# Optimization experiments

Measured on AMD Instinct MI355X. Metric: run time of the kernel, lower is better.

## Reference

```python
import jax, jax.numpy as jnp
import numpy as np

FPS, MS = 7, 256
WIDTHS = [(FPS, 12), (12, 12), (12, 12), (12, 12), (12, 12), (12, 6), (6, 1)]


def setup_inputs() -> dict:
    key = jax.random.key(0)
    keys = jax.random.split(key, 1 + 2 * len(WIDTHS))
    B = 32768
    inp = {"inputs": jax.random.normal(keys[0], (B, MS, FPS), dtype=jnp.float32)}
    for li, (fan_in, fan_out) in enumerate(WIDTHS):
        scale = 1.0 / np.sqrt(fan_in)
        inp[f"W{li}"] = jax.random.uniform(keys[1 + 2 * li], (fan_in, fan_out), dtype=jnp.float32, minval=-scale, maxval=scale)
        inp[f"b{li}"] = jnp.zeros((fan_out,), dtype=jnp.float32)
    return inp


def _mlp(x, Ws, bs):
    # layer 0: linear activation
    h = x @ Ws[0] + bs[0]
    # layers 1-4: relu
    for li in range(1, 5):
        h = jax.nn.relu(h @ Ws[li] + bs[li])
    # layer 5: linear (6 units), layer 6: final linear (1 unit)
    h = h @ Ws[5] + bs[5]
    h = h @ Ws[6] + bs[6]
    return h


def reference(inputs, W0, b0, W1, b1, W2, b2, W3, b3, W4, b4, W5, b5, W6, b6):
    B = inputs.shape[0]
    Ws = [W0, W1, W2, W3, W4, W5, W6]
    bs = [b0, b1, b2, b3, b4, b5, b6]
    # Equivalent to looping over ms slices with the shared MLP then concatenating:
    # fold the ms dim into the batch, run once, reshape back to [B, ms].
    x = inputs.reshape(B * MS, FPS)
    out = _mlp(x, Ws, bs)  # [B*MS, 1]
    return out.reshape(B, MS)
```

## Files before the change

kernel.cpp:

```cpp
#include <hip/hip_runtime.h>
#include <stdint.h>

typedef _Float16 half8  __attribute__((ext_vector_type(8)));
typedef __fp16   fp16x2 __attribute__((ext_vector_type(2)));
typedef float    floatx4 __attribute__((ext_vector_type(4)));
typedef uint32_t u32x4  __attribute__((ext_vector_type(4)));
typedef float    f4a    __attribute__((ext_vector_type(4), aligned(4)));

union FragU { u32x4 v; uint32_t u[4]; half8 h; };
union H2U   { fp16x2 h; uint32_t u; };
union FU    { float f; uint32_t u; };

#define NT 256
#define NBLOCKS 1024
#define NWAVES (NBLOCKS * (NT / 64))
#define ROWS_PER_GITER (NWAVES * 64)

__device__ __forceinline__ uint32_t splitpk(float y) {
    FU a; a.f = y; a.u &= 0xFFFFE000u;
    H2U r; r.h = __builtin_amdgcn_cvt_pkrtz(a.f, y - a.f);
    return r.u;
}

__global__ void build_frags(const float* __restrict__ W0, const float* __restrict__ b0,
                            const float* __restrict__ W1, const float* __restrict__ b1,
                            const float* __restrict__ W2, const float* __restrict__ b2,
                            const float* __restrict__ W3, const float* __restrict__ b3,
                            const float* __restrict__ W4, const float* __restrict__ b4,
                            const float* __restrict__ W5, const float* __restrict__ b5,
                            const float* __restrict__ W6, const float* __restrict__ b6,
                            uint32_t* __restrict__ ws)
{
    const int l = threadIdx.x;
    if (l >= 64) return;
    const int m = l & 15, g = l >> 4;
    const float* Wm[5] = {W0, W1, W2, W3, W4};
    const float* bm[5] = {b0, b1, b2, b3, b4};

    for (int s = 0; s < 6; ++s) {
        const int fan_in = (s == 0) ? 7 : 12;
        const int mmax   = (s == 5) ? 1 : 12;
        const float wscale = (s == 0) ? 64.0f : (s == 5 ? (1.0f / 64.0f) : 1.0f);
        for (int w = 0; w < 4; ++w) {
            const int i = g * 4 + w;
            uint32_t u1 = 0, u2 = 0;
            if (g == 3 && w == 3) {
                float bv = 0.0f;
                if (m < mmax) {
                    if (s == 5) { bv = b6[0]; for (int c = 0; c < 6; ++c) bv = fmaf(b5[c], W6[c], bv); }
                    else        { bv = 64.0f * bm[s][m]; }
                }
                H2U hh; hh.h = __builtin_amdgcn_cvt_pkrtz(bv, 0.0f);
                float hf = (float)hh.h[0];
                H2U ll; ll.h = __builtin_amdgcn_cvt_pkrtz(bv - hf, 0.0f);
                u1 = hh.u; u2 = ll.u;
            } else if (i < fan_in && m < mmax) {
                float wv;
                if (s == 5) { wv = 0.0f; for (int c = 0; c < 6; ++c) wv = fmaf(W5[i * 6 + c], W6[c], wv); wv *= wscale; }
                else        { wv = Wm[s][i * 12 + m] * wscale; }
                H2U hh; hh.h = __builtin_amdgcn_cvt_pkrtz(wv, wv);
                float hf = (float)hh.h[0];
                H2U ll; ll.h = __builtin_amdgcn_cvt_pkrtz(wv - hf, 0.0f);
                u1 = hh.u; u2 = ll.u;
            }
            ws[((s * 2 + 0) * 64 + l) * 4 + w] = u1;
            ws[((s * 2 + 1) * 64 + l) * 4 + w] = u2;
        }
    }
}

__device__ __forceinline__ void mlp16x4(const half8 (&A)[6][2], const f4a (&q)[4],
                                        floatx4 (&acc)[4], bool godd, bool g3)
{
    FragU B[4];
    #pragma unroll
    for (int st = 0; st < 4; ++st) {
        float v0 = godd ? (float)q[st][1] : (float)q[st][0];
        float v1 = godd ? (float)q[st][2] : (float)q[st][1];
        float v2 = godd ? (float)q[st][3] : (float)q[st][2];
        float v3 = godd ? 0.0f           : (float)q[st][3];
        B[st].u[0] = splitpk(v0);
        B[st].u[1] = splitpk(v1);
        B[st].u[2] = splitpk(v2);
        B[st].u[3] = g3 ? 0x00003C00u : splitpk(v3);
    }
    #pragma unroll
    for (int st = 0; st < 4; ++st) {
        floatx4 a = {0.f, 0.f, 0.f, 0.f};
        a = __builtin_amdgcn_mfma_f32_16x16x32_f16(A[0][0], B[st].h, a, 0, 0, 0);
        a = __builtin_amdgcn_mfma_f32_16x16x32_f16(A[0][1], B[st].h, a, 0, 0, 0);
        acc[st] = a;
    }
    #pragma unroll
    for (int s = 1; s <= 5; ++s) {
        #pragma unroll
        for (int st = 0; st < 4; ++st) {
            float y0 = acc[st][0], y1 = acc[st][1], y2 = acc[st][2], y3 = acc[st][3];
            if (s >= 2) {
                y0 = fmaxf(y0, 0.f); y1 = fmaxf(y1, 0.f);
                y2 = fmaxf(y2, 0.f); y3 = fmaxf(y3, 0.f);
            }
            B[st].u[0] = splitpk(y0);
            B[st].u[1] = splitpk(y1);
            B[st].u[2] = splitpk(y2);
            B[st].u[3] = g3 ? 0x00003C00u : splitpk(y3);
        }
        #pragma unroll
        for (int st = 0; st < 4; ++st) {
            floatx4 a = {0.f, 0.f, 0.f, 0.f};
            a = __builtin_amdgcn_mfma_f32_16x16x32_f16(A[s][0], B[st].h, a, 0, 0, 0);
            a = __builtin_amdgcn_mfma_f32_16x16x32_f16(A[s][1], B[st].h, a, 0, 0, 0);
            acc[st] = a;
        }
    }
}

__global__ __launch_bounds__(NT, 4) void mlp_mfma(const float* __restrict__ in,
                                                  const uint32_t* __restrict__ ws,
                                                  float* __restrict__ out, int nrows)
{
    const int tid  = threadIdx.x;
    const int lane = tid & 63;
    const int m = lane & 15, g = lane >> 4;
    const bool godd = (g & 1) != 0;
    const bool g3   = (g == 3);

    half8 A[6][2];
    #pragma unroll
    for (int s = 0; s < 6; ++s)
        #pragma unroll
        for (int f = 0; f < 2; ++f) {
            FragU fu;
            fu.v = *(const u32x4*)(ws + ((s * 2 + f) * 64 + lane) * 4);
            A[s][f] = fu.h;
        }

    const int wid  = (int)blockIdx.x * (NT / 64) + (tid >> 6);
    const int wuid = __builtin_amdgcn_readfirstlane(wid);
    const float* inp = in  + (size_t)wuid * (64 * 7);
    float*      outp = out + (size_t)wuid * 64;
    const int voffx = m * 7 + (godd ? 3 : 0);

    const int niter = nrows / ROWS_PER_GITER;

    for (int t = 0; t < niter; ++t) {
        f4a q[4];
        #pragma unroll
        for (int st = 0; st < 4; ++st)
            q[st] = *(const f4a*)(inp + voffx + st * (16 * 7));

        floatx4 acc[4];
        mlp16x4(A, q, acc, godd, g3);

        if (lane < 16) {
            #pragma unroll
            for (int st = 0; st < 4; ++st)
                outp[st * 16 + m] = acc[st][0];
        }
        inp  += (size_t)ROWS_PER_GITER * 7;
        outp += ROWS_PER_GITER;
    }

    const int done = niter * ROWS_PER_GITER;
    if (done < nrows) {
        const int rowbase = done + wuid * 64;
        if (rowbase < nrows) {
            f4a q[4];
            #pragma unroll
            for (int st = 0; st < 4; ++st) {
                int row = rowbase + st * 16 + m;
                int rowc = row < nrows ? row : nrows - 1;
                q[st] = *(const f4a*)(in + (size_t)rowc * 7 + (godd ? 3 : 0));
            }
            floatx4 acc[4];
            mlp16x4(A, q, acc, godd, g3);
            if (lane < 16) {
                #pragma unroll
                for (int st = 0; st < 4; ++st) {
                    int row = rowbase + st * 16 + m;
                    if (row < nrows) out[row] = acc[st][0];
                }
            }
        }
    }
}

extern "C" void kernel_launch(void* const* d_in, const int* in_sizes, int n_in,
                              void* d_out, int out_size, void* d_ws, size_t ws_size,
                              hipStream_t stream) {
    const float* in = (const float*)d_in[0];
    const float* W0 = (const float*)d_in[1];  const float* b0 = (const float*)d_in[2];
    const float* W1 = (const float*)d_in[3];  const float* b1 = (const float*)d_in[4];
    const float* W2 = (const float*)d_in[5];  const float* b2 = (const float*)d_in[6];
    const float* W3 = (const float*)d_in[7];  const float* b3 = (const float*)d_in[8];
    const float* W4 = (const float*)d_in[9];  const float* b4 = (const float*)d_in[10];
    const float* W5 = (const float*)d_in[11]; const float* b5 = (const float*)d_in[12];
    const float* W6 = (const float*)d_in[13]; const float* b6 = (const float*)d_in[14];
    float* out = (float*)d_out;
    uint32_t* ws = (uint32_t*)d_ws;

    hipLaunchKernelGGL(build_frags, dim3(1), dim3(64), 0, stream,
                       W0, b0, W1, b1, W2, b2, W3, b3, W4, b4, W5, b5, W6, b6, ws);

    const int nrows = in_sizes[0] / 7;
    hipLaunchKernelGGL(mlp_mfma, dim3(NBLOCKS), dim3(NT), 0, stream,
                       in, ws, out, nrows);
}
```

Measured before the change: 141.4 us.

## Double-buffer input loads and fold lane-shift selection into layer-0 weights

Restructures the main loop to prefetch the next iteration's input fragments into a second register buffer while the current tile runs through the MLP, so global load latency overlaps with MFMA work. The odd-group lane shift (selecting q[1..3] vs q[0..2]) is moved into the layer-0 weight fragment layout built once in build_frags, removing per-element selects from the hot path. The per-tile split and MFMA are also interleaved per subtile instead of running in two separate passes. This costs extra VGPRs for the second buffer, which may pressure occupancy under the launch bound of 4.

Result: faster. 132.0 us (-6.7%).

```diff
diff --git a/kernel.cpp b/kernel.cpp
--- a/kernel.cpp
+++ b/kernel.cpp
@@ -42,7 +42,6 @@
         const int mmax   = (s == 5) ? 1 : 12;
         const float wscale = (s == 0) ? 64.0f : (s == 5 ? (1.0f / 64.0f) : 1.0f);
         for (int w = 0; w < 4; ++w) {
-            const int i = g * 4 + w;
             uint32_t u1 = 0, u2 = 0;
             if (g == 3 && w == 3) {
                 float bv = 0.0f;
@@ -54,14 +53,19 @@
                 float hf = (float)hh.h[0];
                 H2U ll; ll.h = __builtin_amdgcn_cvt_pkrtz(bv - hf, 0.0f);
                 u1 = hh.u; u2 = ll.u;
-            } else if (i < fan_in && m < mmax) {
-                float wv;
-                if (s == 5) { wv = 0.0f; for (int c = 0; c < 6; ++c) wv = fmaf(W5[i * 6 + c], W6[c], wv); wv *= wscale; }
-                else        { wv = Wm[s][i * 12 + m] * wscale; }
-                H2U hh; hh.h = __builtin_amdgcn_cvt_pkrtz(wv, wv);
-                float hf = (float)hh.h[0];
-                H2U ll; ll.h = __builtin_amdgcn_cvt_pkrtz(wv - hf, 0.0f);
-                u1 = hh.u; u2 = ll.u;
+            } else {
+                int i; bool ok;
+                if (s == 0) { i = (g & 1) ? 3 + w : w; ok = ((g == 0) || (g == 1 && w > 0)) && (m < mmax); }
+                else        { i = g * 4 + w;           ok = (i < fan_in) && (m < mmax); }
+                if (ok) {
+                    float wv;
+                    if (s == 5) { wv = 0.0f; for (int c = 0; c < 6; ++c) wv = fmaf(W5[i * 6 + c], W6[c], wv); wv *= wscale; }
+                    else        { wv = Wm[s][i * 12 + m] * wscale; }
+                    H2U hh; hh.h = __builtin_amdgcn_cvt_pkrtz(wv, wv);
+                    float hf = (float)hh.h[0];
+                    H2U ll; ll.h = __builtin_amdgcn_cvt_pkrtz(wv - hf, 0.0f);
+                    u1 = hh.u; u2 = ll.u;
+                }
             }
             ws[((s * 2 + 0) * 64 + l) * 4 + w] = u1;
             ws[((s * 2 + 1) * 64 + l) * 4 + w] = u2;
@@ -70,25 +74,19 @@
 }
 
 __device__ __forceinline__ void mlp16x4(const half8 (&A)[6][2], const f4a (&q)[4],
-                                        floatx4 (&acc)[4], bool godd, bool g3)
+                                        floatx4 (&acc)[4], bool g3)
 {
-    FragU B[4];
+    const floatx4 fzero = {0.f, 0.f, 0.f, 0.f};
     #pragma unroll
     for (int st = 0; st < 4; ++st) {
-        float v0 = godd ? (float)q[st][1] : (float)q[st][0];
-        float v1 = godd ? (float)q[st][2] : (float)q[st][1];
-        float v2 = godd ? (float)q[st][3] : (float)q[st][2];
-        float v3 = godd ? 0.0f           : (float)q[st][3];
-        B[st].u[0] = splitpk(v0);
-        B[st].u[1] = splitpk(v1);
-        B[st].u[2] = splitpk(v2);
-        B[st].u[3] = g3 ? 0x00003C00u : splitpk(v3);
-    }
-    #pragma unroll
-    for (int st = 0; st < 4; ++st) {
-        floatx4 a = {0.f, 0.f, 0.f, 0.f};
-        a = __builtin_amdgcn_mfma_f32_16x16x32_f16(A[0][0], B[st].h, a, 0, 0, 0);
-        a = __builtin_amdgcn_mfma_f32_16x16x32_f16(A[0][1], B[st].h, a, 0, 0, 0);
+        FragU B;
+        B.u[0] = splitpk(q[st][0]);
+        B.u[1] = splitpk(q[st][1]);
+        B.u[2] = splitpk(q[st][2]);
+        B.u[3] = g3 ? 0x00003C00u : splitpk(q[st][3]);
+        floatx4 a = fzero;
+        a = __builtin_amdgcn_mfma_f32_16x16x32_f16(A[0][0], B.h, a, 0, 0, 0);
+        a = __builtin_amdgcn_mfma_f32_16x16x32_f16(A[0][1], B.h, a, 0, 0, 0);
         acc[st] = a;
     }
     #pragma unroll
@@ -100,16 +98,14 @@
                 y0 = fmaxf(y0, 0.f); y1 = fmaxf(y1, 0.f);
                 y2 = fmaxf(y2, 0.f); y3 = fmaxf(y3, 0.f);
             }
-            B[st].u[0] = splitpk(y0);
-            B[st].u[1] = splitpk(y1);
-            B[st].u[2] = splitpk(y2);
-            B[st].u[3] = g3 ? 0x00003C00u : splitpk(y3);
-        }
-        #pragma unroll
-        for (int st = 0; st < 4; ++st) {
-            floatx4 a = {0.f, 0.f, 0.f, 0.f};
-            a = __builtin_amdgcn_mfma_f32_16x16x32_f16(A[s][0], B[st].h, a, 0, 0, 0);
-            a = __builtin_amdgcn_mfma_f32_16x16x32_f16(A[s][1], B[st].h, a, 0, 0, 0);
+            FragU B;
+            B.u[0] = splitpk(y0);
+            B.u[1] = splitpk(y1);
+            B.u[2] = splitpk(y2);
+            B.u[3] = g3 ? 0x00003C00u : splitpk(y3);
+            floatx4 a = fzero;
+            a = __builtin_amdgcn_mfma_f32_16x16x32_f16(A[s][0], B.h, a, 0, 0, 0);
+            a = __builtin_amdgcn_mfma_f32_16x16x32_f16(A[s][1], B.h, a, 0, 0, 0);
             acc[st] = a;
         }
     }
@@ -142,23 +138,36 @@
     const int voffx = m * 7 + (godd ? 3 : 0);
 
     const int niter = nrows / ROWS_PER_GITER;
-
-    for (int t = 0; t < niter; ++t) {
-        f4a q[4];
-        #pragma unroll
-        for (int st = 0; st < 4; ++st)
-            q[st] = *(const f4a*)(inp + voffx + st * (16 * 7));
-
-        floatx4 acc[4];
-        mlp16x4(A, q, acc, godd, g3);
-
-        if (lane < 16) {
-            #pragma unroll
-            for (int st = 0; st < 4; ++st)
-                outp[st * 16 + m] = acc[st][0];
-        }
-        inp  += (size_t)ROWS_PER_GITER * 7;
-        outp += ROWS_PER_GITER;
+    const size_t S7 = (size_t)ROWS_PER_GITER * 7;
+
+#define LOADQ(dst, base) { \
+    _Pragma("unroll") \
+    for (int st = 0; st < 4; ++st) dst[st] = *(const f4a*)((base) + voffx + st * (16 * 7)); }
+
+    if (niter > 0) {
+        f4a qa[4], qb[4];
+        LOADQ(qa, inp);
+        for (int t = 0; t < niter; t += 2) {
+            const float* p1 = (t + 1 < niter) ? (inp + S7) : inp;
+            LOADQ(qb, p1);
+            floatx4 acc[4];
+            mlp16x4(A, qa, acc, g3);
+            if (lane < 16) {
+                #pragma unroll
+                for (int st = 0; st < 4; ++st) outp[st * 16 + m] = acc[st][0];
+            }
+            const float* p2 = (t + 2 < niter) ? (inp + 2 * S7) : inp;
+            LOADQ(qa, p2);
+            if (t + 1 < niter) {
+                mlp16x4(A, qb, acc, g3);
+                if (lane < 16) {
+                    #pragma unroll
+                    for (int st = 0; st < 4; ++st) (outp + ROWS_PER_GITER)[st * 16 + m] = acc[st][0];
+                }
+            }
+            inp  += 2 * S7;
+            outp += 2 * (size_t)ROWS_PER_GITER;
+        }
     }
 
     const int done = niter * ROWS_PER_GITER;
@@ -173,7 +182,7 @@
                 q[st] = *(const f4a*)(in + (size_t)rowc * 7 + (godd ? 3 : 0));
             }
             floatx4 acc[4];
-            mlp16x4(A, q, acc, godd, g3);
+            mlp16x4(A, q, acc, g3);
             if (lane < 16) {
                 #pragma unroll
                 for (int st = 0; st < 4; ++st) {
@@ -183,6 +192,7 @@
             }
         }
     }
+#undef LOADQ
 }
 
 extern "C" void kernel_launch(void* const* d_in, const int* in_sizes, int n_in,
```
